# Performance work log

Measured on AMD Instinct MI355X. Metric: run time of the kernel, lower is better.

## Reference

```python
import jax, jax.numpy as jnp
import numpy as np

B, T, D, H = 2, 2048, 1024, 16
DK = D // H  # 64

def setup_inputs() -> dict:
    key = jax.random.key(0)
    ks = jax.random.split(key, 9)
    s = 1.0 / np.sqrt(D)
    return {
        "x": jax.random.normal(ks[0], (B, T, D), dtype=jnp.float32),
        "wq": jax.random.normal(ks[1], (D, D), dtype=jnp.float32) * s,
        "bq": jax.random.normal(ks[2], (D,), dtype=jnp.float32) * 0.01,
        "wk": jax.random.normal(ks[3], (D, D), dtype=jnp.float32) * s,
        "bk": jax.random.normal(ks[4], (D,), dtype=jnp.float32) * 0.01,
        "wv": jax.random.normal(ks[5], (D, D), dtype=jnp.float32) * s,
        "bv": jax.random.normal(ks[6], (D,), dtype=jnp.float32) * 0.01,
        "wo": jax.random.normal(ks[7], (D, D), dtype=jnp.float32) * s,
        "bo": jax.random.normal(ks[8], (D,), dtype=jnp.float32) * 0.01,
    }

def reference(x, wq, bq, wk, bk, wv, bv, wo, bo):
    b, t, d = x.shape
    # projections (torch Linear: y = x @ W^T + b)
    q = (x @ wq.T + bq).reshape(b, t, H, DK).transpose(0, 2, 1, 3)  # [B,H,T,dk]
    k = (x @ wk.T + bk).reshape(b, t, H, DK).transpose(0, 2, 1, 3)
    v = (x @ wv.T + bv).reshape(b, t, H, DK).transpose(0, 2, 1, 3)
    scores = jnp.einsum('bhqd,bhkd->bhqk', q, k) * (1.0 / np.sqrt(DK))
    causal = jnp.tril(jnp.ones((t, t), dtype=bool))
    scores = jnp.where(causal[None, None], scores, -jnp.inf)
    probs = jax.nn.softmax(scores, axis=-1)
    y = jnp.einsum('bhqk,bhkd->bhqd', probs, v)
    y = y.transpose(0, 2, 1, 3).reshape(b, t, d)
    return y @ wo.T + bo
```

## Files before the change

kernel.cpp:

```cpp
#include <hip/hip_runtime.h>
#include <hip/hip_bf16.h>

#define T_SEQ 2048
#define DMODEL 1024
#define NHEAD 16
#define DKH 64
#define BATCH 2

typedef __attribute__((ext_vector_type(8))) short bf16x8;
typedef __attribute__((ext_vector_type(4))) float f32x4;

__device__ inline unsigned short f2bf(float f) {
  unsigned u = __builtin_bit_cast(unsigned, f);
  u += 0x7fffu + ((u >> 16) & 1u);
  return (unsigned short)(u >> 16);
}

#if __has_builtin(__builtin_amdgcn_exp2f)
__device__ inline float fast_exp2(float x) { return __builtin_amdgcn_exp2f(x); }
#else
__device__ inline float fast_exp2(float x) { return exp2f(x); }
#endif

__device__ inline unsigned pack2bf(float a, float b) {
  __hip_bfloat162 t = __float22bfloat162_rn(float2{a, b});
  unsigned r;
  __builtin_memcpy(&r, &t, 4);
  return r;
}

__global__ void castk(const float* __restrict__ in, unsigned short* __restrict__ out, int n) {
  int i = (blockIdx.x * blockDim.x + threadIdx.x) * 4;
  if (i >= n) return;
  float4 v = *reinterpret_cast<const float4*>(in + i);
  ushort4 o;
  o.x = f2bf(v.x); o.y = f2bf(v.y); o.z = f2bf(v.z); o.w = f2bf(v.w);
  *reinterpret_cast<ushort4*>(out + i) = o;
}

__global__ void castw(const float* __restrict__ wq, const float* __restrict__ wk,
                      const float* __restrict__ wv, const float* __restrict__ wo,
                      unsigned short* __restrict__ Wqkv, unsigned short* __restrict__ Wob,
                      float qscale) {
  const int NW = DMODEL * DMODEL;
  int i = (blockIdx.x * blockDim.x + threadIdx.x) * 4;
  if (i >= 4 * NW) return;
  if (i < 3 * NW) {
    const float* src; float sc = 1.0f; int off = i;
    if (i < NW) { src = wq; sc = qscale; }
    else if (i < 2 * NW) { src = wk; off = i - NW; }
    else { src = wv; off = i - 2 * NW; }
    float4 v = *reinterpret_cast<const float4*>(src + off);
    ushort4 o;
    o.x = f2bf(v.x * sc); o.y = f2bf(v.y * sc); o.z = f2bf(v.z * sc); o.w = f2bf(v.w * sc);
    *reinterpret_cast<ushort4*>(Wqkv + i) = o;
  } else {
    int off = i - 3 * NW;
    float4 v = *reinterpret_cast<const float4*>(wo + off);
    ushort4 o;
    o.x = f2bf(v.x); o.y = f2bf(v.y); o.z = f2bf(v.z); o.w = f2bf(v.w);
    *reinterpret_cast<ushort4*>(Wob + off) = o;
  }
}

__global__ __launch_bounds__(256) void gemm_qkv(
    const unsigned short* __restrict__ A,
    const unsigned short* __restrict__ Bw,
    const float* __restrict__ bq,
    const float* __restrict__ bk,
    const float* __restrict__ bv,
    unsigned short* __restrict__ Qb,
    unsigned short* __restrict__ Kb,
    unsigned short* __restrict__ Vtb,
    int K, float qscale)
{
  __shared__ __attribute__((aligned(16))) unsigned short As[64][72];
  __shared__ __attribute__((aligned(16))) unsigned short Bs[64][72];
  const int tid = threadIdx.x;
  const int lane = tid & 63, wid = tid >> 6;
  const int wm = (wid >> 1) * 32, wn = (wid & 1) * 32;
  const int lr = lane & 15, lk = (lane >> 4) * 8, lg = lane >> 4;
  const int bm = blockIdx.y * 64, bn = blockIdx.x * 64;
  const int srow = tid >> 3, scol = (tid & 7) * 8;

  f32x4 acc[2][2] = {};
  for (int k0 = 0; k0 < K; k0 += 64) {
    uint4 a0 = *reinterpret_cast<const uint4*>(&A[(size_t)(bm + srow) * K + k0 + scol]);
    uint4 a1 = *reinterpret_cast<const uint4*>(&A[(size_t)(bm + srow + 32) * K + k0 + scol]);
    uint4 b0 = *reinterpret_cast<const uint4*>(&Bw[(size_t)(bn + srow) * K + k0 + scol]);
    uint4 b1 = *reinterpret_cast<const uint4*>(&Bw[(size_t)(bn + srow + 32) * K + k0 + scol]);
    *reinterpret_cast<uint4*>(&As[srow][scol]) = a0;
    *reinterpret_cast<uint4*>(&As[srow + 32][scol]) = a1;
    *reinterpret_cast<uint4*>(&Bs[srow][scol]) = b0;
    *reinterpret_cast<uint4*>(&Bs[srow + 32][scol]) = b1;
    __syncthreads();
#pragma unroll
    for (int kc = 0; kc < 64; kc += 32) {
      bf16x8 fa0 = *reinterpret_cast<const bf16x8*>(&As[wm + lr][kc + lk]);
      bf16x8 fa1 = *reinterpret_cast<const bf16x8*>(&As[wm + 16 + lr][kc + lk]);
      bf16x8 fb0 = *reinterpret_cast<const bf16x8*>(&Bs[wn + lr][kc + lk]);
      bf16x8 fb1 = *reinterpret_cast<const bf16x8*>(&Bs[wn + 16 + lr][kc + lk]);
      acc[0][0] = __builtin_amdgcn_mfma_f32_16x16x32_bf16(fa0, fb0, acc[0][0], 0, 0, 0);
      acc[0][1] = __builtin_amdgcn_mfma_f32_16x16x32_bf16(fa0, fb1, acc[0][1], 0, 0, 0);
      acc[1][0] = __builtin_amdgcn_mfma_f32_16x16x32_bf16(fa1, fb0, acc[1][0], 0, 0, 0);
      acc[1][1] = __builtin_amdgcn_mfma_f32_16x16x32_bf16(fa1, fb1, acc[1][1], 0, 0, 0);
    }
    __syncthreads();
  }

  const int sec = bn >> 10;
#pragma unroll
  for (int i = 0; i < 2; ++i)
#pragma unroll
    for (int j = 0; j < 2; ++j) {
      const int nbase = bn + wn + j * 16 + lr;
      const int d = nbase & (DMODEL - 1), hh = d >> 6, dk = d & 63;
      const float bval = (sec == 0) ? bq[d] * qscale : ((sec == 1) ? bk[d] : bv[d]);
      if (sec == 2) {
        const int m0 = bm + wm + i * 16 + lg * 4;
        const int bb = m0 >> 11, tp = m0 & (T_SEQ - 1);
        ushort4 o;
        o.x = f2bf(acc[i][j][0] + bval);
        o.y = f2bf(acc[i][j][1] + bval);
        o.z = f2bf(acc[i][j][2] + bval);
        o.w = f2bf(acc[i][j][3] + bval);
        *reinterpret_cast<ushort4*>(
            &Vtb[(size_t)((bb * NHEAD + hh) * DKH + dk) * T_SEQ + tp]) = o;
      } else {
        unsigned short* dst = (sec == 0) ? Qb : Kb;
#pragma unroll
        for (int t = 0; t < 4; ++t) {
          const int m = bm + wm + i * 16 + lg * 4 + t;
          const int bb = m >> 11, tp = m & (T_SEQ - 1);
          dst[(size_t)((bb * NHEAD + hh) * T_SEQ + tp) * DKH + dk] = f2bf(acc[i][j][t] + bval);
        }
      }
    }
}

__global__ __launch_bounds__(256) void gemm_out(
    const unsigned short* __restrict__ A,
    const unsigned short* __restrict__ Bw,
    const float* __restrict__ bias,
    float* __restrict__ outp,
    int N, int K)
{
  __shared__ __attribute__((aligned(16))) unsigned short As[64][72];
  __shared__ __attribute__((aligned(16))) unsigned short Bs[64][72];
  const int tid = threadIdx.x;
  const int lane = tid & 63, wid = tid >> 6;
  const int wm = (wid >> 1) * 32, wn = (wid & 1) * 32;
  const int lr = lane & 15, lk = (lane >> 4) * 8, lg = lane >> 4;
  const int bm = blockIdx.y * 64, bn = blockIdx.x * 64;
  const int srow = tid >> 3, scol = (tid & 7) * 8;

  f32x4 acc[2][2] = {};
  for (int k0 = 0; k0 < K; k0 += 64) {
    uint4 a0 = *reinterpret_cast<const uint4*>(&A[(size_t)(bm + srow) * K + k0 + scol]);
    uint4 a1 = *reinterpret_cast<const uint4*>(&A[(size_t)(bm + srow + 32) * K + k0 + scol]);
    uint4 b0 = *reinterpret_cast<const uint4*>(&Bw[(size_t)(bn + srow) * K + k0 + scol]);
    uint4 b1 = *reinterpret_cast<const uint4*>(&Bw[(size_t)(bn + srow + 32) * K + k0 + scol]);
    *reinterpret_cast<uint4*>(&As[srow][scol]) = a0;
    *reinterpret_cast<uint4*>(&As[srow + 32][scol]) = a1;
    *reinterpret_cast<uint4*>(&Bs[srow][scol]) = b0;
    *reinterpret_cast<uint4*>(&Bs[srow + 32][scol]) = b1;
    __syncthreads();
#pragma unroll
    for (int kc = 0; kc < 64; kc += 32) {
      bf16x8 fa0 = *reinterpret_cast<const bf16x8*>(&As[wm + lr][kc + lk]);
      bf16x8 fa1 = *reinterpret_cast<const bf16x8*>(&As[wm + 16 + lr][kc + lk]);
      bf16x8 fb0 = *reinterpret_cast<const bf16x8*>(&Bs[wn + lr][kc + lk]);
      bf16x8 fb1 = *reinterpret_cast<const bf16x8*>(&Bs[wn + 16 + lr][kc + lk]);
      acc[0][0] = __builtin_amdgcn_mfma_f32_16x16x32_bf16(fa0, fb0, acc[0][0], 0, 0, 0);
      acc[0][1] = __builtin_amdgcn_mfma_f32_16x16x32_bf16(fa0, fb1, acc[0][1], 0, 0, 0);
      acc[1][0] = __builtin_amdgcn_mfma_f32_16x16x32_bf16(fa1, fb0, acc[1][0], 0, 0, 0);
      acc[1][1] = __builtin_amdgcn_mfma_f32_16x16x32_bf16(fa1, fb1, acc[1][1], 0, 0, 0);
    }
    __syncthreads();
  }

#pragma unroll
  for (int i = 0; i < 2; ++i)
#pragma unroll
    for (int j = 0; j < 2; ++j) {
      const int nbase = bn + wn + j * 16 + lr;
      const float bval = bias[nbase];
#pragma unroll
      for (int t = 0; t < 4; ++t) {
        const int m = bm + wm + i * 16 + lg * 4 + t;
        outp[(size_t)m * N + nbase] = acc[i][j][t] + bval;
      }
    }
}

__global__ __launch_bounds__(256, 2) void attn_k(
    const unsigned short* __restrict__ Q,
    const unsigned short* __restrict__ K,
    const unsigned short* __restrict__ Vt,
    unsigned short* __restrict__ Yb)
{
  __shared__ float Ol[4][64][68];
  __shared__ float Lp[4][64];
  const int tid = threadIdx.x;
  const int lane = tid & 63, w = tid >> 6;
  const int lr = lane & 15, g = lane >> 4;
  const int bh = blockIdx.y, b = bh >> 4, h = bh & 15;
  const int bq = (T_SEQ / 64 - 1) - blockIdx.x;
  const int q0 = bq * 64;
  const int nt = bq + 1, last = nt - 1;

  const unsigned short* Qb = Q + (size_t)bh * T_SEQ * DKH;
  const unsigned short* Kb = K + (size_t)bh * T_SEQ * DKH;
  const unsigned short* Vb = Vt + (size_t)bh * DKH * T_SEQ;

  bf16x8 qa[4][2];
#pragma unroll
  for (int qf4 = 0; qf4 < 4; ++qf4)
#pragma unroll
    for (int kk = 0; kk < 2; ++kk)
      qa[qf4][kk] = *reinterpret_cast<const bf16x8*>(
          &Qb[(size_t)(q0 + qf4 * 16 + lr) * DKH + kk * 32 + g * 8]);

  f32x4 o[4][4] = {};
  float lsum[4] = {0.f, 0.f, 0.f, 0.f};

  auto tile = [&](int k0, bool masked) {
    bf16x8 ka[4][2];
#pragma unroll
    for (int f = 0; f < 4; ++f)
#pragma unroll
      for (int kk = 0; kk < 2; ++kk)
        ka[f][kk] = *reinterpret_cast<const bf16x8*>(
            &Kb[(size_t)(k0 + f * 16 + lr) * DKH + kk * 32 + g * 8]);

    bf16x8 vf[4][2];
#pragma unroll
    for (int df = 0; df < 4; ++df)
#pragma unroll
      for (int kk = 0; kk < 2; ++kk)
        vf[df][kk] = *reinterpret_cast<const bf16x8*>(
            &Vb[(size_t)(df * 16 + lr) * T_SEQ + k0 + kk * 32 + g * 8]);

#pragma unroll
    for (int qp = 0; qp < 2; ++qp) {
      f32x4 s[2][4] = {};
#pragma unroll
      for (int f = 0; f < 4; ++f) {
        s[0][f] = __builtin_amdgcn_mfma_f32_16x16x32_bf16(ka[f][0], qa[2 * qp][0], s[0][f], 0, 0, 0);
        s[0][f] = __builtin_amdgcn_mfma_f32_16x16x32_bf16(ka[f][1], qa[2 * qp][1], s[0][f], 0, 0, 0);
        s[1][f] = __builtin_amdgcn_mfma_f32_16x16x32_bf16(ka[f][0], qa[2 * qp + 1][0], s[1][f], 0, 0, 0);
        s[1][f] = __builtin_amdgcn_mfma_f32_16x16x32_bf16(ka[f][1], qa[2 * qp + 1][1], s[1][f], 0, 0, 0);
      }

      unsigned pk[2][4][2];
#pragma unroll
      for (int qf = 0; qf < 2; ++qf)
#pragma unroll
        for (int f = 0; f < 4; ++f) {
          float p[4];
#pragma unroll
          for (int r = 0; r < 4; ++r) {
            float sv = s[qf][f][r];
            if (masked)
              sv = (k0 + f * 16 + g * 4 + r <= q0 + (2 * qp + qf) * 16 + lr) ? sv : -1e30f;
            p[r] = fast_exp2(sv);
          }
          lsum[2 * qp + qf] += (p[0] + p[1]) + (p[2] + p[3]);
          pk[qf][f][0] = pack2bf(p[0], p[1]);
          pk[qf][f][1] = pack2bf(p[2], p[3]);
        }

      const int sA = lr + 16 * (2 * (g & 1));
      const int sB = sA + 16;
#pragma unroll
      for (int qf = 0; qf < 2; ++qf)
#pragma unroll
        for (int kk = 0; kk < 2; ++kk) {
          int dw[4];
#pragma unroll
          for (int j2 = 0; j2 < 4; ++j2) {
            const int S = (j2 < 2) ? sA : sB;
            int v0 = __shfl((int)pk[qf][2 * kk][j2 & 1], S, 64);
            int v1 = __shfl((int)pk[qf][2 * kk + 1][j2 & 1], S, 64);
            dw[j2] = (g & 2) ? v1 : v0;
          }
          int4 dwi = make_int4(dw[0], dw[1], dw[2], dw[3]);
          bf16x8 pa = __builtin_bit_cast(bf16x8, dwi);
#pragma unroll
          for (int df = 0; df < 4; ++df)
            o[2 * qp + qf][df] = __builtin_amdgcn_mfma_f32_16x16x32_bf16(
                vf[df][kk], pa, o[2 * qp + qf][df], 0, 0, 0);
        }
    }
  };

  for (int t = w; t < last; t += 4) tile(t * 64, false);
  if (last >= 0 && (last & 3) == w) tile(last * 64, true);

#pragma unroll
  for (int qf4 = 0; qf4 < 4; ++qf4) {
    lsum[qf4] += __shfl_xor(lsum[qf4], 16);
    lsum[qf4] += __shfl_xor(lsum[qf4], 32);
  }

#pragma unroll
  for (int qf4 = 0; qf4 < 4; ++qf4) {
    if (g == 0) Lp[w][qf4 * 16 + lr] = lsum[qf4];
#pragma unroll
    for (int df = 0; df < 4; ++df)
      *reinterpret_cast<f32x4*>(&Ol[w][qf4 * 16 + lr][df * 16 + g * 4]) = o[qf4][df];
  }
  __syncthreads();

  const int ql = tid >> 2, d0 = (tid & 3) * 16;
  const float l = Lp[0][ql] + Lp[1][ql] + Lp[2][ql] + Lp[3][ql];
  const float rl = 1.0f / l;
  float sacc[16] = {};
#pragma unroll
  for (int w2 = 0; w2 < 4; ++w2)
#pragma unroll
    for (int c4 = 0; c4 < 4; ++c4) {
      f32x4 a = *reinterpret_cast<const f32x4*>(&Ol[w2][ql][d0 + c4 * 4]);
      sacc[c4 * 4 + 0] += a[0]; sacc[c4 * 4 + 1] += a[1];
      sacc[c4 * 4 + 2] += a[2]; sacc[c4 * 4 + 3] += a[3];
    }
  uint4 ov0, ov1;
  ov0.x = pack2bf(sacc[0] * rl,  sacc[1] * rl);
  ov0.y = pack2bf(sacc[2] * rl,  sacc[3] * rl);
  ov0.z = pack2bf(sacc[4] * rl,  sacc[5] * rl);
  ov0.w = pack2bf(sacc[6] * rl,  sacc[7] * rl);
  ov1.x = pack2bf(sacc[8] * rl,  sacc[9] * rl);
  ov1.y = pack2bf(sacc[10] * rl, sacc[11] * rl);
  ov1.z = pack2bf(sacc[12] * rl, sacc[13] * rl);
  ov1.w = pack2bf(sacc[14] * rl, sacc[15] * rl);
  unsigned short* yrow = &Yb[(size_t)(b * T_SEQ + q0 + ql) * DMODEL + h * DKH + d0];
  *reinterpret_cast<uint4*>(yrow) = ov0;
  *reinterpret_cast<uint4*>(yrow + 8) = ov1;
}

extern "C" void kernel_launch(void* const* d_in, const int* in_sizes, int n_in,
                              void* d_out, int out_size, void* d_ws, size_t ws_size,
                              hipStream_t stream) {
  const float* x  = (const float*)d_in[0];
  const float* wq = (const float*)d_in[1];
  const float* bq = (const float*)d_in[2];
  const float* wk = (const float*)d_in[3];
  const float* bk = (const float*)d_in[4];
  const float* wv = (const float*)d_in[5];
  const float* bv = (const float*)d_in[6];
  const float* wo = (const float*)d_in[7];
  const float* bo = (const float*)d_in[8];

  char* ws = (char*)d_ws;
  unsigned short* xb   = (unsigned short*)(ws + (size_t)0);
  unsigned short* Wqkv = (unsigned short*)(ws + ((size_t)8  << 20));
  unsigned short* Wob  = (unsigned short*)(ws + ((size_t)14 << 20));
  unsigned short* Qb   = (unsigned short*)(ws + ((size_t)16 << 20));
  unsigned short* Kb   = (unsigned short*)(ws + ((size_t)24 << 20));
  unsigned short* Vtb  = (unsigned short*)(ws + ((size_t)32 << 20));
  unsigned short* Yb   = (unsigned short*)(ws + ((size_t)40 << 20));

  const int M = BATCH * T_SEQ;
  const int N = DMODEL;
  const int Kd = DMODEL;
  const float qscale = 0.125f * 1.44269504f;

  castk<<<(M * DMODEL) / 1024, 256, 0, stream>>>(x, xb, M * DMODEL);
  castw<<<(DMODEL * DMODEL) / 256, 256, 0, stream>>>(wq, wk, wv, wo, Wqkv, Wob, qscale);

  gemm_qkv<<<dim3(3 * N / 64, M / 64), 256, 0, stream>>>(
      xb, Wqkv, bq, bk, bv, Qb, Kb, Vtb, Kd, qscale);

  attn_k<<<dim3(T_SEQ / 64, BATCH * NHEAD), 256, 0, stream>>>(Qb, Kb, Vtb, Yb);

  gemm_out<<<dim3(N / 64, M / 64), 256, 0, stream>>>(Yb, Wob, bo, (float*)d_out, N, Kd);
}
```

Measured before the change: 148.3 us.

## Prefetch next K tile in registers and swizzle attention block order

The attention kernel now loads the next K tile (four tiles ahead, per wave) into registers right after the QK MFMAs of the current tile. This overlaps global K loads with the softmax and PV work, replacing the lambda that loaded K at the start of each tile. The launch grid is flattened to 1D with a block-index swizzle that spreads consecutive blocks over eight groups, so adjacent work-groups get varied query-tile lengths and heads. This aims to balance causal work across CUs and XCDs, at the cost of extra live registers that may reduce occupancy.

```diff
diff --git a/kernel.cpp b/kernel.cpp
--- a/kernel.cpp
+++ b/kernel.cpp
@@ -204,8 +204,11 @@
   const int tid = threadIdx.x;
   const int lane = tid & 63, w = tid >> 6;
   const int lr = lane & 15, g = lane >> 4;
-  const int bh = blockIdx.y, b = bh >> 4, h = bh & 15;
-  const int bq = (T_SEQ / 64 - 1) - blockIdx.x;
+  const int bid = blockIdx.x;
+  const int swz = ((bid & 7) << 7) | (bid >> 3);
+  const int bh = swz >> 5;
+  const int bq = (T_SEQ / 64 - 1) - (swz & 31);
+  const int b = bh >> 4, h = bh & 15;
   const int q0 = bq * 64;
   const int nt = bq + 1, last = nt - 1;
 
@@ -224,14 +227,20 @@
   f32x4 o[4][4] = {};
   float lsum[4] = {0.f, 0.f, 0.f, 0.f};
 
-  auto tile = [&](int k0, bool masked) {
-    bf16x8 ka[4][2];
+  bf16x8 ka[4][2];
+  if (w <= last) {
 #pragma unroll
     for (int f = 0; f < 4; ++f)
 #pragma unroll
       for (int kk = 0; kk < 2; ++kk)
         ka[f][kk] = *reinterpret_cast<const bf16x8*>(
-            &Kb[(size_t)(k0 + f * 16 + lr) * DKH + kk * 32 + g * 8]);
+            &Kb[(size_t)(w * 64 + f * 16 + lr) * DKH + kk * 32 + g * 8]);
+  }
+
+  for (int t = w; t <= last; t += 4) {
+    const int k0 = t * 64;
+    const bool masked = (t == last);
+    const bool pref = (t + 4 <= last);
 
     bf16x8 vf[4][2];
 #pragma unroll
@@ -250,6 +259,15 @@
         s[0][f] = __builtin_amdgcn_mfma_f32_16x16x32_bf16(ka[f][1], qa[2 * qp][1], s[0][f], 0, 0, 0);
         s[1][f] = __builtin_amdgcn_mfma_f32_16x16x32_bf16(ka[f][0], qa[2 * qp + 1][0], s[1][f], 0, 0, 0);
         s[1][f] = __builtin_amdgcn_mfma_f32_16x16x32_bf16(ka[f][1], qa[2 * qp + 1][1], s[1][f], 0, 0, 0);
+      }
+
+      if (qp == 1 && pref) {
+#pragma unroll
+        for (int f = 0; f < 4; ++f)
+#pragma unroll
+          for (int kk = 0; kk < 2; ++kk)
+            ka[f][kk] = *reinterpret_cast<const bf16x8*>(
+                &Kb[(size_t)(k0 + 256 + f * 16 + lr) * DKH + kk * 32 + g * 8]);
       }
 
       unsigned pk[2][4][2];
@@ -292,10 +310,7 @@
                 vf[df][kk], pa, o[2 * qp + qf][df], 0, 0, 0);
         }
     }
-  };
-
-  for (int t = w; t < last; t += 4) tile(t * 64, false);
-  if (last >= 0 && (last & 3) == w) tile(last * 64, true);
+  }
 
 #pragma unroll
   for (int qf4 = 0; qf4 < 4; ++qf4) {
@@ -371,7 +386,7 @@
   gemm_qkv<<<dim3(3 * N / 64, M / 64), 256, 0, stream>>>(
       xb, Wqkv, bq, bk, bv, Qb, Kb, Vtb, Kd, qscale);
 
-  attn_k<<<dim3(T_SEQ / 64, BATCH * NHEAD), 256, 0, stream>>>(Qb, Kb, Vtb, Yb);
+  attn_k<<<dim3((T_SEQ / 64) * BATCH * NHEAD), 256, 0, stream>>>(Qb, Kb, Vtb, Yb);
 
   gemm_out<<<dim3(N / 64, M / 64), 256, 0, stream>>>(Yb, Wob, bo, (float*)d_out, N, Kd);
 }
```

Result: slower. 153.2 us (+3.3%).
